# Optimization experiments

Hardware: AMD Instinct MI355X
Metric: run time of the kernel (lower is better)

## Reference

```python
import jax, jax.numpy as jnp
import numpy as np

T, D, H, E = 8192, 1024, 512, 8
BLK = 32  # MXFP8 scaling block size along the contraction dim


def setup_inputs() -> dict:
    key = jax.random.key(0)
    k1, k2, k3, k4 = jax.random.split(key, 4)
    # qdata: values representable-ish in e4m3 (we use small normal floats)
    output_e4m3 = jax.random.normal(k1, (T, D), dtype=jnp.float32)
    # e8m0 scales are powers of two, one per 32-element block along dim
    output_scales_e8m0 = jnp.exp2(
        jax.random.randint(k2, (T, D // BLK), -2, 3).astype(jnp.float32)
    )
    # uniform token distribution across experts (tokens are expert-contiguous)
    num_tokens_per_expert = jnp.full((E,), T // E, dtype=jnp.int32)
    expert_padded_offsets = jnp.zeros((E,), dtype=jnp.int32)  # unused by forward body
    w13 = jax.random.normal(k3, (E, 2 * H, D), dtype=jnp.float32) * 0.02
    w2 = jax.random.normal(k4, (E, D, H), dtype=jnp.float32) * 0.02
    return {
        "output_e4m3": output_e4m3,
        "output_scales_e8m0": output_scales_e8m0,
        "num_tokens_per_expert": num_tokens_per_expert,
        "expert_padded_offsets": expert_padded_offsets,
        "w13": w13,
        "w2": w2,
    }


def reference(output_e4m3, output_scales_e8m0, num_tokens_per_expert,
              expert_padded_offsets, w13, w2):
    # Dequantize MXFP8: qdata * per-block e8m0 scale, blocks of 32 along dim.
    scales = jnp.repeat(output_scales_e8m0, BLK, axis=-1)  # [T, D]
    x = output_e4m3 * scales  # [T, D] high-precision reference activations
    # Grouped GEMM 1: tokens are expert-contiguous with uniform group sizes,
    # so the ragged grouped matmul reduces to a batched einsum per expert.
    tpe = T // E
    xg = x.reshape(E, tpe, D)                       # [E, tpe, D]
    h13 = jnp.einsum("etd,ehd->eth", xg, w13)       # [E, tpe, 2H]
    h1, h3 = h13[..., :H], h13[..., H:]
    h = jax.nn.silu(h1) * h3                        # fused SiLU-gate
    # Grouped GEMM 2
    out = jnp.einsum("eth,edh->etd", h, w2)         # [E, tpe, D]
    return out.reshape(T, D)
```

## Files before the change

### kernel.cpp

```cpp
#include <hip/hip_runtime.h>
#include <hip/hip_bf16.h>

#define T_TOK 8192
#define DDIM  1024
#define HDIM  512
#define NE    8
#define TPE   (T_TOK / NE)

typedef __attribute__((ext_vector_type(4))) float floatx4;
typedef __attribute__((ext_vector_type(8))) short bf16x8;

#define SBAR() __builtin_amdgcn_sched_barrier(0)

__device__ __forceinline__ unsigned short f2bf(float f) {
    union { float f; unsigned int u; } v;
    v.f = f;
    unsigned int u = v.u;
    unsigned int r = u + 0x7FFFu + ((u >> 16) & 1u);
    return (unsigned short)(r >> 16);
}

__device__ __forceinline__ unsigned int cvt_pk_bf16(float lo, float hi) {
    unsigned int r;
    asm("v_cvt_pk_bf16_f32 %0, %1, %2" : "=v"(r) : "v"(lo), "v"(hi));
    return r;
}

__device__ __forceinline__ void gld_lds16(const void* g, void* l) {
    __builtin_amdgcn_global_load_lds(
        (const __attribute__((address_space(1))) unsigned int*)g,
        (__attribute__((address_space(3))) unsigned int*)l, 16, 0, 0);
}

__global__ __launch_bounds__(256)
void convert_x_kernel(const float* __restrict__ X, const float* __restrict__ S,
                      unsigned short* __restrict__ Xb)
{
    const int NTX = (T_TOK * DDIM) / 4;
    const int stride = gridDim.x * blockDim.x;
    for (int i = blockIdx.x * blockDim.x + threadIdx.x; i < NTX; i += stride) {
        int row = i >> 8;
        int c4  = i & 255;
        float4 v = reinterpret_cast<const float4*>(X)[i];
        float sc = S[row * (DDIM / 32) + (c4 >> 3)];
        ushort4 b;
        b.x = f2bf(v.x * sc); b.y = f2bf(v.y * sc);
        b.z = f2bf(v.z * sc); b.w = f2bf(v.w * sc);
        reinterpret_cast<ushort4*>(Xb)[i] = b;
    }
}

__device__ __forceinline__ int xcd_swizzle_512(int raw) {
    return (raw & 7) * 64 + (raw >> 3);
}
__device__ __forceinline__ int xcd_swizzle_256(int raw) {
    return (raw & 7) * 32 + (raw >> 3);
}


__global__ __launch_bounds__(512, 2)
void gemm1_silu_kernel(const unsigned short* __restrict__ Xb,
                       const float* __restrict__ W13,
                       __hip_bfloat16* __restrict__ Hout)
{
    const int bid = xcd_swizzle_256(blockIdx.x);
    const int e  = bid >> 5;
    const int mt = (bid >> 3) & 3;
    const int nt = bid & 7;
    const int tok0 = e * TPE + mt * 256;
    const float* __restrict__ We = W13 + (size_t)e * (2 * HDIM) * DDIM;

    __shared__ __hip_bfloat16 sA[2][256][64];
    __shared__ __hip_bfloat16 sB[2][128][64];

    const int tid  = threadIdx.x;
    const int lane = tid & 63;
    const int wave = tid >> 6;
    const int wr = wave >> 1;
    const int wc = wave & 1;
    const int lr = lane & 15;
    const int sw0 = ((lane >> 4) ^ (lane & 7));

    floatx4 acc1[4][2] = {};
    floatx4 acc3[4][2] = {};

    const int srowA = tid >> 3;
    const int dcolA = (tid & 7) * 8;
    const int gcolA = ((tid & 7) ^ (srowA & 7)) * 8;
    const int srowB = tid >> 4;
    const int f4    = tid & 15;
    const int bcol  = f4 * 4;

    float4 rB0[4], rB1[4];

    auto LOADB = [&](int kk, float4* rB) {
        const int k0 = kk * 64;
        #pragma unroll
        for (int j = 0; j < 4; ++j) {
            int row = srowB + j * 32;
            int wrow = (j < 2) ? (nt * 64 + row)
                               : (HDIM + nt * 64 + (row - 64));
            rB[j] = *reinterpret_cast<const float4*>(
                        &We[(size_t)wrow * DDIM + k0 + bcol]);
        }
    };
    auto STAGEA = [&](int kk, int buf) {
        const int k0 = kk * 64;
        #pragma unroll
        for (int j = 0; j < 4; ++j) {
            int row = srowA + j * 64;
            gld_lds16(&Xb[(size_t)(tok0 + row) * DDIM + k0 + gcolA],
                      &sA[buf][row][dcolA]);
        }
    };
    auto WRITEB = [&](int buf, const float4* rB) {
        #pragma unroll
        for (int j = 0; j < 4; ++j) {
            int row = srowB + j * 32;
            uint2 w;
            w.x = cvt_pk_bf16(rB[j].x, rB[j].y);
            w.y = cvt_pk_bf16(rB[j].z, rB[j].w);
            char* base = reinterpret_cast<char*>(&sB[buf][row][0]);
            int off = (((f4 >> 1) ^ (row & 7)) << 4) + ((f4 & 1) << 3);
            *reinterpret_cast<uint2*>(base + off) = w;
        }
    };
    auto COMPUTE_KS = [&](int buf, int ks) {
        const int rc = (sw0 ^ (ks << 2)) << 3;
        bf16x8 a[4], b1[2], b3[2];
        #pragma unroll
        for (int m = 0; m < 4; ++m)
            a[m] = *reinterpret_cast<const bf16x8*>(&sA[buf][wr * 64 + m * 16 + lr][rc]);
        #pragma unroll
        for (int n = 0; n < 2; ++n) {
            b1[n] = *reinterpret_cast<const bf16x8*>(&sB[buf][wc * 32 + n * 16 + lr][rc]);
            b3[n] = *reinterpret_cast<const bf16x8*>(&sB[buf][64 + wc * 32 + n * 16 + lr][rc]);
        }
        #pragma unroll
        for (int m = 0; m < 4; ++m)
            #pragma unroll
            for (int n = 0; n < 2; ++n) {
                acc1[m][n] = __builtin_amdgcn_mfma_f32_16x16x32_bf16(a[m], b1[n], acc1[m][n], 0, 0, 0);
                acc3[m][n] = __builtin_amdgcn_mfma_f32_16x16x32_bf16(a[m], b3[n], acc3[m][n], 0, 0, 0);
            }
    };

    LOADB(0, rB0);  SBAR();
    STAGEA(0, 0);   SBAR();
    LOADB(1, rB1);  SBAR();
    asm volatile("s_waitcnt vmcnt(8)" ::: "memory");
    SBAR();
    WRITEB(0, rB0); SBAR();
    asm volatile("s_waitcnt vmcnt(4) lgkmcnt(0)" ::: "memory");
    SBAR();
    __builtin_amdgcn_s_barrier();

    for (int t = 0; t < DDIM / 64 - 2; t += 2) {
        STAGEA(t + 1, 1);   SBAR();
        LOADB(t + 2, rB0);  SBAR();
        COMPUTE_KS(0, 0);
        COMPUTE_KS(0, 1);
        asm volatile("s_waitcnt vmcnt(8)" ::: "memory");
        SBAR();
        WRITEB(1, rB1);     SBAR();
        asm volatile("s_waitcnt vmcnt(4) lgkmcnt(0)" ::: "memory");
        SBAR();
        __builtin_amdgcn_s_barrier();
        STAGEA(t + 2, 0);   SBAR();
        LOADB(t + 3, rB1);  SBAR();
        COMPUTE_KS(1, 0);
        COMPUTE_KS(1, 1);
        asm volatile("s_waitcnt vmcnt(8)" ::: "memory");
        SBAR();
        WRITEB(0, rB0);     SBAR();
        asm volatile("s_waitcnt vmcnt(4) lgkmcnt(0)" ::: "memory");
        SBAR();
        __builtin_amdgcn_s_barrier();
    }

    STAGEA(15, 1);    SBAR();
    COMPUTE_KS(0, 0);
    COMPUTE_KS(0, 1);
    asm volatile("s_waitcnt vmcnt(4)" ::: "memory");
    SBAR();
    WRITEB(1, rB1);   SBAR();
    asm volatile("s_waitcnt vmcnt(0) lgkmcnt(0)" ::: "memory");
    SBAR();
    __builtin_amdgcn_s_barrier();
    COMPUTE_KS(1, 0);
    COMPUTE_KS(1, 1);

    const int hcol0 = nt * 64 + wc * 32;
    #pragma unroll
    for (int m = 0; m < 4; ++m) {
        #pragma unroll
        for (int n = 0; n < 2; ++n) {
            #pragma unroll
            for (int i = 0; i < 4; ++i) {
                int row = tok0 + wr * 64 + m * 16 + (lane >> 4) * 4 + i;
                int col = hcol0 + n * 16 + (lane & 15);
                float h1 = acc1[m][n][i];
                float h3 = acc3[m][n][i];
                float sig = 1.0f / (1.0f + __expf(-h1));
                Hout[(size_t)row * HDIM + col] = __float2bfloat16(h1 * sig * h3);
            }
        }
    }
}

__global__ __launch_bounds__(256, 2)
void gemm2_kernel(const __hip_bfloat16* __restrict__ Hin,
                  const float* __restrict__ W2,
                  float* __restrict__ Out)
{
    const int bid = xcd_swizzle_512(blockIdx.x);
    const int e  = bid >> 6;
    const int nt = (bid >> 3) & 7;
    const int mt = bid & 7;
    const int tok0 = e * TPE + mt * 128;
    const float* __restrict__ We = W2 + (size_t)e * DDIM * HDIM;

    __shared__ __hip_bfloat16 sA[2][128][64];
    __shared__ __hip_bfloat16 sB[2][128][64];

    const int tid  = threadIdx.x;
    const int lane = tid & 63;
    const int wave = tid >> 6;
    const int wr = wave >> 1;
    const int wc = wave & 1;
    const int lr = lane & 15;
    const int sw0 = ((lane >> 4) ^ (lane & 7));

    floatx4 acc[4][4] = {};

    const int srow0 = (tid >> 3);
    const int c8    = (tid & 7) * 8;
    const int dcol  = (tid & 7) * 8;
    const int swcol = ((tid & 7) ^ (srow0 & 7)) * 8;

    float4 rB0[8], rB1[8];

    auto LOADB = [&](int kk, float4* rB) {
        const int k0 = kk * 64;
        #pragma unroll
        for (int j = 0; j < 4; ++j) {
            int row = srow0 + j * 32;
            const float* p = &We[(size_t)(nt * 128 + row) * HDIM + k0 + c8];
            rB[2*j]   = *reinterpret_cast<const float4*>(p);
            rB[2*j+1] = *reinterpret_cast<const float4*>(p + 4);
        }
    };
    auto STAGEA = [&](int kk, int buf) {
        const int k0 = kk * 64;
        #pragma unroll
        for (int j = 0; j < 4; ++j) {
            int row = srow0 + j * 32;
            gld_lds16(&Hin[(size_t)(tok0 + row) * HDIM + k0 + swcol],
                      &sA[buf][row][dcol]);
        }
    };
    auto WRITEB = [&](int buf, const float4* rB) {
        #pragma unroll
        for (int j = 0; j < 4; ++j) {
            int row = srow0 + j * 32;
            uint4 w;
            w.x = cvt_pk_bf16(rB[2*j].x,   rB[2*j].y);
            w.y = cvt_pk_bf16(rB[2*j].z,   rB[2*j].w);
            w.z = cvt_pk_bf16(rB[2*j+1].x, rB[2*j+1].y);
            w.w = cvt_pk_bf16(rB[2*j+1].z, rB[2*j+1].w);
            *reinterpret_cast<uint4*>(&sB[buf][row][swcol]) = w;
        }
    };
    auto COMPUTE = [&](int buf) {
        #pragma unroll
        for (int ks = 0; ks < 2; ++ks) {
            const int rc = (sw0 ^ (ks << 2)) << 3;
            bf16x8 a[4], b[4];
            #pragma unroll
            for (int m = 0; m < 4; ++m)
                a[m] = *reinterpret_cast<const bf16x8*>(&sA[buf][wr * 64 + m * 16 + lr][rc]);
            #pragma unroll
            for (int n = 0; n < 4; ++n)
                b[n] = *reinterpret_cast<const bf16x8*>(&sB[buf][wc * 64 + n * 16 + lr][rc]);
            #pragma unroll
            for (int m = 0; m < 4; ++m)
                #pragma unroll
                for (int n = 0; n < 4; ++n)
                    acc[m][n] = __builtin_amdgcn_mfma_f32_16x16x32_bf16(a[m], b[n], acc[m][n], 0, 0, 0);
        }
    };

    LOADB(0, rB0);  SBAR();
    STAGEA(0, 0);   SBAR();
    LOADB(1, rB1);  SBAR();
    asm volatile("s_waitcnt vmcnt(12)" ::: "memory");
    SBAR();
    WRITEB(0, rB0); SBAR();
    asm volatile("s_waitcnt vmcnt(8) lgkmcnt(0)" ::: "memory");
    SBAR();
    __builtin_amdgcn_s_barrier();

    for (int t = 0; t < HDIM / 64 - 2; t += 2) {
        STAGEA(t + 1, 1);   SBAR();
        LOADB(t + 2, rB0);  SBAR();
        COMPUTE(0);
        asm volatile("s_waitcnt vmcnt(12)" ::: "memory");
        SBAR();
        WRITEB(1, rB1);     SBAR();
        asm volatile("s_waitcnt vmcnt(8) lgkmcnt(0)" ::: "memory");
        SBAR();
        __builtin_amdgcn_s_barrier();
        STAGEA(t + 2, 0);   SBAR();
        LOADB(t + 3, rB1);  SBAR();
        COMPUTE(1);
        asm volatile("s_waitcnt vmcnt(12)" ::: "memory");
        SBAR();
        WRITEB(0, rB0);     SBAR();
        asm volatile("s_waitcnt vmcnt(8) lgkmcnt(0)" ::: "memory");
        SBAR();
        __builtin_amdgcn_s_barrier();
    }

    STAGEA(7, 1);   SBAR();
    COMPUTE(0);
    asm volatile("s_waitcnt vmcnt(4)" ::: "memory");
    SBAR();
    WRITEB(1, rB1); SBAR();
    asm volatile("s_waitcnt vmcnt(0) lgkmcnt(0)" ::: "memory");
    SBAR();
    __builtin_amdgcn_s_barrier();
    COMPUTE(1);

    const int dcol0 = nt * 128 + wc * 64;
    #pragma unroll
    for (int m = 0; m < 4; ++m) {
        #pragma unroll
        for (int n = 0; n < 4; ++n) {
            #pragma unroll
            for (int i = 0; i < 4; ++i) {
                int row = tok0 + wr * 64 + m * 16 + (lane >> 4) * 4 + i;
                int col = dcol0 + n * 16 + (lane & 15);
                Out[(size_t)row * DDIM + col] = acc[m][n][i];
            }
        }
    }
}

extern "C" void kernel_launch(void* const* d_in, const int* in_sizes, int n_in,
                              void* d_out, int out_size, void* d_ws, size_t ws_size,
                              hipStream_t stream) {
    const float* X   = (const float*)d_in[0];
    const float* S   = (const float*)d_in[1];
    const float* W13 = (const float*)d_in[4];
    const float* W2  = (const float*)d_in[5];
    float* Out = (float*)d_out;

    __hip_bfloat16* Hb = (__hip_bfloat16*)d_ws;
    unsigned short* Xb = (unsigned short*)d_out;

    convert_x_kernel<<<2048, 256, 0, stream>>>(X, S, Xb);
    gemm1_silu_kernel<<<NE * 4 * 8, 512, 0, stream>>>(Xb, W13, Hb);
    gemm2_kernel<<<NE * 8 * 8, 256, 0, stream>>>(Hb, W2, Out);
}
```

Before: 54.49 us.

## Interleave LDS reads, global staging and MFMA clusters with ping-pong barriers and setprio

```diff
diff --git a/kernel.cpp b/kernel.cpp
--- a/kernel.cpp
+++ b/kernel.cpp
@@ -11,6 +11,8 @@
 typedef __attribute__((ext_vector_type(8))) short bf16x8;
 
 #define SBAR() __builtin_amdgcn_sched_barrier(0)
+#define BARRIER() __builtin_amdgcn_s_barrier()
+#define WAIT_LGKM0() do { asm volatile("s_waitcnt lgkmcnt(0)" ::: "memory"); SBAR(); } while (0)
 
 __device__ __forceinline__ unsigned short f2bf(float f) {
     union { float f; unsigned int u; } v;
@@ -125,25 +127,40 @@
             *reinterpret_cast<uint2*>(base + off) = w;
         }
     };
-    auto COMPUTE_KS = [&](int buf, int ks) {
+    auto DS_A = [&](int buf, int ks, bf16x8* a) {
         const int rc = (sw0 ^ (ks << 2)) << 3;
-        bf16x8 a[4], b1[2], b3[2];
         #pragma unroll
         for (int m = 0; m < 4; ++m)
             a[m] = *reinterpret_cast<const bf16x8*>(&sA[buf][wr * 64 + m * 16 + lr][rc]);
-        #pragma unroll
-        for (int n = 0; n < 2; ++n) {
-            b1[n] = *reinterpret_cast<const bf16x8*>(&sB[buf][wc * 32 + n * 16 + lr][rc]);
-            b3[n] = *reinterpret_cast<const bf16x8*>(&sB[buf][64 + wc * 32 + n * 16 + lr][rc]);
-        }
+    };
+    auto DS_B1 = [&](int buf, int ks, bf16x8* b) {
+        const int rc = (sw0 ^ (ks << 2)) << 3;
+        #pragma unroll
+        for (int n = 0; n < 2; ++n)
+            b[n] = *reinterpret_cast<const bf16x8*>(&sB[buf][wc * 32 + n * 16 + lr][rc]);
+    };
+    auto DS_B3 = [&](int buf, int ks, bf16x8* b) {
+        const int rc = (sw0 ^ (ks << 2)) << 3;
+        #pragma unroll
+        for (int n = 0; n < 2; ++n)
+            b[n] = *reinterpret_cast<const bf16x8*>(&sB[buf][64 + wc * 32 + n * 16 + lr][rc]);
+    };
+    auto MFMA1 = [&](bf16x8* a, bf16x8* b) {
         #pragma unroll
         for (int m = 0; m < 4; ++m)
             #pragma unroll
-            for (int n = 0; n < 2; ++n) {
-                acc1[m][n] = __builtin_amdgcn_mfma_f32_16x16x32_bf16(a[m], b1[n], acc1[m][n], 0, 0, 0);
-                acc3[m][n] = __builtin_amdgcn_mfma_f32_16x16x32_bf16(a[m], b3[n], acc3[m][n], 0, 0, 0);
-            }
-    };
+            for (int n = 0; n < 2; ++n)
+                acc1[m][n] = __builtin_amdgcn_mfma_f32_16x16x32_bf16(a[m], b[n], acc1[m][n], 0, 0, 0);
+    };
+    auto MFMA3 = [&](bf16x8* a, bf16x8* b) {
+        #pragma unroll
+        for (int m = 0; m < 4; ++m)
+            #pragma unroll
+            for (int n = 0; n < 2; ++n)
+                acc3[m][n] = __builtin_amdgcn_mfma_f32_16x16x32_bf16(a[m], b[n], acc3[m][n], 0, 0, 0);
+    };
+
+    bf16x8 a[4], a2[4], b1[2], b3[2];
 
     LOADB(0, rB0);  SBAR();
     STAGEA(0, 0);   SBAR();
@@ -153,42 +170,81 @@
     WRITEB(0, rB0); SBAR();
     asm volatile("s_waitcnt vmcnt(4) lgkmcnt(0)" ::: "memory");
     SBAR();
-    __builtin_amdgcn_s_barrier();
+    BARRIER();
 
     for (int t = 0; t < DDIM / 64 - 2; t += 2) {
-        STAGEA(t + 1, 1);   SBAR();
-        LOADB(t + 2, rB0);  SBAR();
-        COMPUTE_KS(0, 0);
-        COMPUTE_KS(0, 1);
-        asm volatile("s_waitcnt vmcnt(8)" ::: "memory");
-        SBAR();
-        WRITEB(1, rB1);     SBAR();
-        asm volatile("s_waitcnt vmcnt(4) lgkmcnt(0)" ::: "memory");
-        SBAR();
-        __builtin_amdgcn_s_barrier();
-        STAGEA(t + 2, 0);   SBAR();
-        LOADB(t + 3, rB1);  SBAR();
-        COMPUTE_KS(1, 0);
-        COMPUTE_KS(1, 1);
-        asm volatile("s_waitcnt vmcnt(8)" ::: "memory");
-        SBAR();
-        WRITEB(0, rB0);     SBAR();
-        asm volatile("s_waitcnt vmcnt(4) lgkmcnt(0)" ::: "memory");
-        SBAR();
-        __builtin_amdgcn_s_barrier();
+        DS_A(0, 0, a); DS_B1(0, 0, b1); SBAR();
+        STAGEA(t + 1, 1); SBAR();
+        BARRIER(); WAIT_LGKM0();
+        __builtin_amdgcn_s_setprio(1); MFMA1(a, b1); __builtin_amdgcn_s_setprio(0);
+        SBAR(); BARRIER();
+        DS_B3(0, 0, b3); SBAR();
+        LOADB(t + 2, rB0); SBAR();
+        BARRIER(); WAIT_LGKM0();
+        __builtin_amdgcn_s_setprio(1); MFMA3(a, b3); __builtin_amdgcn_s_setprio(0);
+        SBAR(); BARRIER();
+        DS_A(0, 1, a2); DS_B1(0, 1, b1); SBAR();
+        asm volatile("s_waitcnt vmcnt(8)" ::: "memory"); SBAR();
+        WRITEB(1, rB1); SBAR();
+        BARRIER(); WAIT_LGKM0();
+        __builtin_amdgcn_s_setprio(1); MFMA1(a2, b1); __builtin_amdgcn_s_setprio(0);
+        SBAR(); BARRIER();
+        DS_B3(0, 1, b3); SBAR();
+        asm volatile("s_waitcnt vmcnt(4)" ::: "memory"); SBAR();
+        BARRIER(); WAIT_LGKM0();
+        __builtin_amdgcn_s_setprio(1); MFMA3(a2, b3); __builtin_amdgcn_s_setprio(0);
+        SBAR(); BARRIER();
+
+        DS_A(1, 0, a); DS_B1(1, 0, b1); SBAR();
+        STAGEA(t + 2, 0); SBAR();
+        BARRIER(); WAIT_LGKM0();
+        __builtin_amdgcn_s_setprio(1); MFMA1(a, b1); __builtin_amdgcn_s_setprio(0);
+        SBAR(); BARRIER();
+        DS_B3(1, 0, b3); SBAR();
+        LOADB(t + 3, rB1); SBAR();
+        BARRIER(); WAIT_LGKM0();
+        __builtin_amdgcn_s_setprio(1); MFMA3(a, b3); __builtin_amdgcn_s_setprio(0);
+        SBAR(); BARRIER();
+        DS_A(1, 1, a2); DS_B1(1, 1, b1); SBAR();
+        asm volatile("s_waitcnt vmcnt(8)" ::: "memory"); SBAR();
+        WRITEB(0, rB0); SBAR();
+        BARRIER(); WAIT_LGKM0();
+        __builtin_amdgcn_s_setprio(1); MFMA1(a2, b1); __builtin_amdgcn_s_setprio(0);
+        SBAR(); BARRIER();
+        DS_B3(1, 1, b3); SBAR();
+        asm volatile("s_waitcnt vmcnt(4)" ::: "memory"); SBAR();
+        BARRIER(); WAIT_LGKM0();
+        __builtin_amdgcn_s_setprio(1); MFMA3(a2, b3); __builtin_amdgcn_s_setprio(0);
+        SBAR(); BARRIER();
     }
 
-    STAGEA(15, 1);    SBAR();
-    COMPUTE_KS(0, 0);
-    COMPUTE_KS(0, 1);
-    asm volatile("s_waitcnt vmcnt(4)" ::: "memory");
-    SBAR();
-    WRITEB(1, rB1);   SBAR();
-    asm volatile("s_waitcnt vmcnt(0) lgkmcnt(0)" ::: "memory");
-    SBAR();
-    __builtin_amdgcn_s_barrier();
-    COMPUTE_KS(1, 0);
-    COMPUTE_KS(1, 1);
+    DS_A(0, 0, a); DS_B1(0, 0, b1); SBAR();
+    STAGEA(15, 1); SBAR();
+    BARRIER(); WAIT_LGKM0();
+    __builtin_amdgcn_s_setprio(1); MFMA1(a, b1); __builtin_amdgcn_s_setprio(0);
+    SBAR(); BARRIER();
+    DS_B3(0, 0, b3); SBAR();
+    BARRIER(); WAIT_LGKM0();
+    __builtin_amdgcn_s_setprio(1); MFMA3(a, b3); __builtin_amdgcn_s_setprio(0);
+    SBAR(); BARRIER();
+    DS_A(0, 1, a2); DS_B1(0, 1, b1); SBAR();
+    asm volatile("s_waitcnt vmcnt(4)" ::: "memory"); SBAR();
+    WRITEB(1, rB1); SBAR();
+    BARRIER(); WAIT_LGKM0();
+    __builtin_amdgcn_s_setprio(1); MFMA1(a2, b1); __builtin_amdgcn_s_setprio(0);
+    SBAR(); BARRIER();
+    DS_B3(0, 1, b3); SBAR();
+    asm volatile("s_waitcnt vmcnt(0)" ::: "memory"); SBAR();
+    BARRIER(); WAIT_LGKM0();
+    __builtin_amdgcn_s_setprio(1); MFMA3(a2, b3); __builtin_amdgcn_s_setprio(0);
+    SBAR(); BARRIER();
+
+    DS_A(1, 0, a); DS_B1(1, 0, b1); DS_B3(1, 0, b3);
+    WAIT_LGKM0();
+    MFMA1(a, b1); MFMA3(a, b3);
+    DS_A(1, 1, a2); DS_B1(1, 1, b1); DS_B3(1, 1, b3);
+    WAIT_LGKM0();
+    MFMA1(a2, b1); MFMA3(a2, b3);
 
     const int hcol0 = nt * 64 + wc * 32;
     #pragma unroll
```

Measured after the change: 55.25 us. No clear change (+1.4%).
